# Optimization experiments

Hardware: AMD Instinct MI355X
Metric: run time of the kernel (lower is better)

The kernel has to match this reference:

```python
import jax, jax.numpy as jnp
import numpy as np

NUM_NODES = 19
RESOLUTION = 256
K_KNN = 3
EDGE_TOP_PERC = 0.5
RESIDUAL_W = 0.1
HIDDEN = 128
INPUT_DIM = 32


def _w(k, shape, fan):
    return jax.random.normal(k, shape, jnp.float32) / np.sqrt(fan)


def setup_inputs() -> dict:
    key = jax.random.key(0)
    ks = jax.random.split(key, 12)
    D, H = INPUT_DIM, HIDDEN
    return {
        "x": jax.random.normal(ks[0], (16 * NUM_NODES, 2048, D), jnp.float32),
        # GRU layer 0 (pytorch gate order r,z,n)
        "Wih0": _w(ks[1], (3 * H, D), D), "Whh0": _w(ks[2], (3 * H, H), H),
        "bih0": jnp.zeros(3 * H, jnp.float32), "bhh0": jnp.zeros(3 * H, jnp.float32),
        # GRU layer 1
        "Wih1": _w(ks[3], (3 * H, H), H), "Whh1": _w(ks[4], (3 * H, H), H),
        "bih1": jnp.zeros(3 * H, jnp.float32), "bhh1": jnp.zeros(3 * H, jnp.float32),
        # self-attention graph learner
        "Wq": _w(ks[5], (H, H), H), "Wk": _w(ks[6], (H, H), H),
        # SAGEConv: lin_l (neighbors, with bias) + lin_r (root)
        "Wl": _w(ks[7], (H, H), H), "Wr": _w(ks[8], (H, H), H),
        "b_sage": jnp.zeros(H, jnp.float32),
        # classifier
        "Wc": _w(ks[9], (1, H), H), "bc": jnp.zeros(1, jnp.float32),
    }


def gru_layer(x, Wih, Whh, bih, bhh):
    """x: (B,T,D) -> (B,T,H), pytorch nn.GRU gate order (r,z,n)."""
    H = Whh.shape[1]

    def step(h, xt):
        gi = xt @ Wih.T + bih          # (B,3H)
        gh = h @ Whh.T + bhh
        i_r, i_z, i_n = jnp.split(gi, 3, axis=-1)
        h_r, h_z, h_n = jnp.split(gh, 3, axis=-1)
        r = jax.nn.sigmoid(i_r + h_r)
        z = jax.nn.sigmoid(i_z + h_z)
        n = jnp.tanh(i_n + r * h_n)
        h_new = (1.0 - z) * n + z * h
        return h_new, h_new

    h0 = jnp.zeros((x.shape[0], H), x.dtype)
    _, ys = jax.lax.scan(step, h0, jnp.swapaxes(x, 0, 1))
    return jnp.swapaxes(ys, 0, 1)


def graphs4mer_forward(x, Wih0, Whh0, bih0, bhh0, Wih1, Whh1, bih1, bhh1,
                       Wq, Wk, Wl, Wr, b_sage, Wc, bc):
    B_total, T, _ = x.shape
    batch = B_total // NUM_NODES
    # temporal model: 2-layer GRU
    h = gru_layer(x, Wih0, Whh0, bih0, bhh0)
    h = gru_layer(h, Wih1, Whh1, bih1, bhh1)
    H = h.shape[-1]
    num_dyn = T // RESOLUTION
    # (batch, N, T, H) -> mean over each resolution window -> (batch, num_dyn, N, H)
    h = h.reshape(batch, NUM_NODES, num_dyn, RESOLUTION, H).mean(axis=3)
    xg = jnp.transpose(h, (0, 2, 1, 3)).reshape(batch * num_dyn, NUM_NODES, H)

    Bp, N = xg.shape[0], NUM_NODES
    I = jnp.eye(N, dtype=xg.dtype)

    # --- KNN cosine graph ---
    xn = xg / jnp.linalg.norm(xg, axis=-1, keepdims=True)
    sim = jnp.einsum('bnd,bmd->bnm', xn, xn)
    knn_val, knn_ind = jax.lax.top_k(sim, K_KNN)
    bi = jnp.arange(Bp)[:, None, None]
    ri = jnp.arange(N)[None, :, None]
    adj_knn = jnp.zeros_like(sim).at[bi, ri, knn_ind].set(knn_val)
    adj_knn = jnp.maximum(adj_knn, 0.0)
    adj_knn = (adj_knn + adj_knn.swapaxes(1, 2)) * 0.5   # undirected
    adj_knn = adj_knn * (1.0 - I) + I                    # force diag = 1

    # --- self-attention graph learner ---
    q = xg @ Wq.T
    k = xg @ Wk.T
    attn = jax.nn.softmax(jnp.einsum('bnd,bmd->bnm', q, k) / np.sqrt(H).astype(np.float32), axis=-1)
    attn = (attn + attn.swapaxes(1, 2)) * 0.5

    adj = RESIDUAL_W * adj_knn + (1.0 - RESIDUAL_W) * attn

    # --- prune: keep top edge_top_perc of entries per graph ---
    Kcut = int(N * N * EDGE_TOP_PERC)
    sorted_desc = -jnp.sort(-adj.reshape(Bp, -1), axis=-1)
    thr = sorted_desc[:, Kcut][:, None, None]
    adj = jnp.where(adj > thr, adj, 0.0)

    # --- feature smoothing regularization: tr(X^T L X)/F^2 ---
    d = adj.sum(-1)
    dis = jnp.where(d > 0, d ** -0.5, 0.0)
    L = I - dis[:, :, None] * adj * dis[:, None, :]
    mat = jnp.einsum('bnf,bnm,bmg->bfg', xg, L, xg) / float(H ** 2)
    reg = jnp.einsum('bff->b', mat).mean()

    # --- GraphSAGE conv on pruned graph (self loops removed, mean aggregation) ---
    adj_ns = adj * (1.0 - I)
    mask = (adj_ns > 0).astype(xg.dtype)
    deg = jnp.maximum(mask.sum(-1, keepdims=True), 1.0)
    agg = jnp.einsum('bnm,bmd->bnd', mask, xg) / deg
    out = jax.nn.relu(agg @ Wl.T + b_sage + xg @ Wr.T)

    # temporal mean pool over dynamic graphs, sum pool over nodes, classify
    out = out.reshape(batch, num_dyn, N, H).mean(axis=1).sum(axis=1)
    logits = out @ Wc.T + bc
    return logits, reg


def reference(x, Wih0, Whh0, bih0, bhh0, Wih1, Whh1, bih1, bhh1,
              Wq, Wk, Wl, Wr, b_sage, Wc, bc):
    return graphs4mer_forward(x, Wih0, Whh0, bih0, bhh0, Wih1, Whh1, bih1, bhh1,
                              Wq, Wk, Wl, Wr, b_sage, Wc, bc)
```

## Files before the change

### kernel.cpp

```cpp
#include <hip/hip_runtime.h>
#include <hip/hip_bf16.h>


#define NSEQ   304
#define TT     2048
#define HH     128
#define NNODE  19
#define NDYN   8
#define NGRAPH 128
#define NBLK   76

typedef __bf16 bf16x8 __attribute__((ext_vector_type(8)));
typedef float  f32x4  __attribute__((ext_vector_type(4)));

static __device__ __forceinline__ f32x4 mfma16(bf16x8 a, bf16x8 b, f32x4 c) {
  return __builtin_amdgcn_mfma_f32_16x16x32_bf16(a, b, c, 0, 0, 0);
}

static __device__ __forceinline__ float gate_step(
    float cr, float cz, float cn, float cm,
    float nBr, float nBz, float bin, float bhn, float hp)
{
  const float er = __builtin_amdgcn_exp2f(__builtin_fmaf(cr, -1.4426950408889634f, nBr));
  const float ez = __builtin_amdgcn_exp2f(__builtin_fmaf(cz, -1.4426950408889634f, nBz));
  const float r  = __builtin_amdgcn_rcpf(1.f + er);
  const float z  = __builtin_amdgcn_rcpf(1.f + ez);
  const float gn = __builtin_fmaf(r, cm + bhn, cn + bin);
  const float en = __builtin_amdgcn_exp2f(gn * 2.8853900817779268f);
  const float nn = __builtin_fmaf(__builtin_amdgcn_rcpf(1.f + en), -2.f, 1.f);
  return __builtin_fmaf(z, hp - nn, nn);
}

__global__ void wprep_kernel(const float* __restrict__ src, __bf16* __restrict__ dst,
                             int K, int nk)
{
  const int i = blockIdx.x * 256 + threadIdx.x;
  const int total = 8 * 3 * nk * 64;
  if (i >= total) return;
  const int l = i & 63;
  int rest = i >> 6;
  const int kc = rest % nk; rest /= nk;
  const int gs = rest % 3;
  const int w  = rest / 3;
  const int row = 128 * gs + 16 * w + (l & 15);
  const float* s = src + (size_t)row * K + kc * 32 + (l >> 4) * 8;
  bf16x8 v;
  #pragma unroll
  for (int u = 0; u < 8; ++u) v[u] = (__bf16)s[u];
  *(bf16x8*)&dst[(size_t)i * 8] = v;
}

__global__ void xprep_kernel(const float* __restrict__ x, __bf16* __restrict__ xb)
{
  const int i = blockIdx.x * 256 + threadIdx.x;
  if (i >= NNODE * TT * 64) return;
  const int l = i & 63;
  const int t = (i >> 6) & (TT - 1);
  const int g = i >> 17;
  const float* s = x + ((size_t)(g * 16 + (l & 15)) * TT + t) * 32 + (l >> 4) * 8;
  bf16x8 v;
  #pragma unroll
  for (int u = 0; u < 8; ++u) v[u] = (__bf16)s[u];
  *(bf16x8*)&xb[(size_t)i * 8] = v;
}

#define STEP_BARRIER() do {                                          \
    asm volatile("s_waitcnt lgkmcnt(0)" ::: "memory");               \
    __builtin_amdgcn_s_barrier();                                    \
    __builtin_amdgcn_sched_barrier(0);                               \
  } while (0)

template<int Q0>
static __device__ __forceinline__ void gru_body(
    const __bf16* __restrict__ xb,
    const __bf16* __restrict__ wI0, const __bf16* __restrict__ wH0,
    const __bf16* __restrict__ wI1, const __bf16* __restrict__ wH1,
    const float* __restrict__ bih0, const float* __restrict__ bhh0,
    const float* __restrict__ bih1, const float* __restrict__ bhh1,
    float* __restrict__ xg,
    __bf16* s0a, __bf16* s0b, __bf16* s1a, __bf16* s1b, int gg)
{
  const int tid = threadIdx.x;
  const int w   = tid >> 6;
  const int l   = tid & 63;
  const int lm  = l & 15;
  const int lq  = l >> 4;
  const int j   = 16 * w + lm;
  const f32x4 z4 = {0.f, 0.f, 0.f, 0.f};

  bf16x8 bI0[3], bH0[3][4], bI1[3][4], bH1[3][4];
  #pragma unroll
  for (int gs = 0; gs < 3; ++gs)
    bI0[gs] = *(const bf16x8*)&wI0[(size_t)((w * 3 + gs) * 64 + l) * 8];
  #pragma unroll
  for (int gs = 0; gs < 3; ++gs)
    #pragma unroll
    for (int kc = 0; kc < 4; ++kc) {
      const size_t fi = (size_t)(((w * 3 + gs) * 4 + kc) * 64 + l) * 8;
      bH0[gs][kc] = *(const bf16x8*)&wH0[fi];
      bI1[gs][kc] = *(const bf16x8*)&wI1[fi];
      bH1[gs][kc] = *(const bf16x8*)&wH1[fi];
    }

  const float L2E = 1.4426950408889634f;
  const float nBr0 = -L2E * (bih0[j] + bhh0[j]);
  const float nBz0 = -L2E * (bih0[128 + j] + bhh0[128 + j]);
  const float bin0 = bih0[256 + j], bhn0 = bhh0[256 + j];
  const float nBr1 = -L2E * (bih1[j] + bhh1[j]);
  const float nBz1 = -L2E * (bih1[128 + j] + bhh1[128 + j]);
  const float bin1 = bih1[256 + j], bhn1 = bhh1[256 + j];

  for (int i = tid; i < 16 * HH; i += 512) {
    s0a[i] = (__bf16)0.f; s0b[i] = (__bf16)0.f;
    s1a[i] = (__bf16)0.f; s1b[i] = (__bf16)0.f;
  }

  const int sw = lm & 7;
  int eo[4];
  #pragma unroll
  for (int kc = 0; kc < 4; ++kc)
    eo[kc] = lm * HH + ((((kc << 2) | lq) ^ sw) << 3);

  const int myrow = lq * 4 + Q0;
  const int woff  = myrow * HH + (((j >> 3) ^ (myrow & 7)) << 3) + (j & 7);
  const int seq   = gg * 16 + myrow;
  const int bidx  = seq / NNODE;
  const int node  = seq - bidx * NNODE;

  float h0p = 0.f, h1p = 0.f, hsum = 0.f;

  const __bf16* xrow = xb + (size_t)gg * TT * 512 + l * 8;
  bf16x8 a0 = *(const bf16x8*)xrow;
  __syncthreads();

  for (int t = 0; t < TT; ++t) {
    __bf16*       h0w = (t & 1) ? s0b : s0a;
    const __bf16* h0r = (t & 1) ? s0a : s0b;
    __bf16*       h1w = (t & 1) ? s1a : s1b;
    const __bf16* h1r = (t & 1) ? s1b : s1a;

    bf16x8 a0n = *(const bf16x8*)(xrow + (size_t)((t + 1) & (TT - 1)) * 512);

    bf16x8 ah0[4], ah1[4];
    #pragma unroll
    for (int kc = 0; kc < 4; ++kc) ah0[kc] = *(const bf16x8*)&h0r[eo[kc]];
    #pragma unroll
    for (int kc = 0; kc < 4; ++kc) ah1[kc] = *(const bf16x8*)&h1r[eo[kc]];

    f32x4 Cr = mfma16(a0, bI0[0], z4);
    f32x4 Cz = mfma16(a0, bI0[1], z4);
    f32x4 Cn = mfma16(a0, bI0[2], z4);

    f32x4 Dr = z4, Dz = z4, Dn = z4, Dm = z4;
    if (t > 0) {
      #pragma unroll
      for (int kc = 0; kc < 4; ++kc) {
        Dr = mfma16(ah0[kc], bI1[0][kc], Dr);
        Dz = mfma16(ah0[kc], bI1[1][kc], Dz);
        Dn = mfma16(ah0[kc], bI1[2][kc], Dn);
      }
      #pragma unroll
      for (int kc = 0; kc < 4; ++kc) {
        Dr = mfma16(ah1[kc], bH1[0][kc], Dr);
        Dz = mfma16(ah1[kc], bH1[1][kc], Dz);
        Dm = mfma16(ah1[kc], bH1[2][kc], Dm);
      }
    }

    f32x4 Cm = z4;
    #pragma unroll
    for (int kc = 0; kc < 4; ++kc) {
      Cr = mfma16(ah0[kc], bH0[0][kc], Cr);
      Cz = mfma16(ah0[kc], bH0[1][kc], Cz);
      Cm = mfma16(ah0[kc], bH0[2][kc], Cm);
    }

    if (t > 0) {
      const float h = gate_step(Dr[Q0], Dz[Q0], Dn[Q0], Dm[Q0],
                                nBr1, nBz1, bin1, bhn1, h1p);
      h1p = h;
      hsum += h;
      h1w[woff] = (__bf16)h;
      const int s = t - 1;
      if ((s & 255) == 255) {
        const int win = s >> 8;
        xg[((size_t)(bidx * NDYN + win) * NNODE + node) * HH + j] =
            hsum * (1.f / 256.f);
        hsum = 0.f;
      }
    }
    {
      const float h = gate_step(Cr[Q0], Cz[Q0], Cn[Q0], Cm[Q0],
                                nBr0, nBz0, bin0, bhn0, h0p);
      h0p = h;
      h0w[woff] = (__bf16)h;
    }
    a0 = a0n;
    STEP_BARRIER();
  }

  {
    const __bf16* h0r = s0b;
    const __bf16* h1r = s1a;
    bf16x8 ah0[4], ah1[4];
    #pragma unroll
    for (int kc = 0; kc < 4; ++kc) ah0[kc] = *(const bf16x8*)&h0r[eo[kc]];
    #pragma unroll
    for (int kc = 0; kc < 4; ++kc) ah1[kc] = *(const bf16x8*)&h1r[eo[kc]];
    f32x4 Dr = z4, Dz = z4, Dn = z4, Dm = z4;
    #pragma unroll
    for (int kc = 0; kc < 4; ++kc) {
      Dr = mfma16(ah0[kc], bI1[0][kc], Dr);
      Dz = mfma16(ah0[kc], bI1[1][kc], Dz);
      Dn = mfma16(ah0[kc], bI1[2][kc], Dn);
    }
    #pragma unroll
    for (int kc = 0; kc < 4; ++kc) {
      Dr = mfma16(ah1[kc], bH1[0][kc], Dr);
      Dz = mfma16(ah1[kc], bH1[1][kc], Dz);
      Dm = mfma16(ah1[kc], bH1[2][kc], Dm);
    }
    const float h = gate_step(Dr[Q0], Dz[Q0], Dn[Q0], Dm[Q0],
                              nBr1, nBz1, bin1, bhn1, h1p);
    hsum += h;
    xg[((size_t)(bidx * NDYN + 7) * NNODE + node) * HH + j] =
        hsum * (1.f / 256.f);
  }
}

__global__ __launch_bounds__(512) __attribute__((amdgpu_waves_per_eu(2, 2)))
void gru2_kernel(
    const __bf16* __restrict__ xb,
    const __bf16* __restrict__ wI0, const __bf16* __restrict__ wH0,
    const __bf16* __restrict__ wI1, const __bf16* __restrict__ wH1,
    const float* __restrict__ bih0, const float* __restrict__ bhh0,
    const float* __restrict__ bih1, const float* __restrict__ bhh1,
    float* __restrict__ xg)
{
  __shared__ __align__(16) __bf16 sH0[2][16 * HH];
  __shared__ __align__(16) __bf16 sH1[2][16 * HH];
  const int gg = blockIdx.x >> 2;
  switch (blockIdx.x & 3) {
    case 0: gru_body<0>(xb, wI0, wH0, wI1, wH1, bih0, bhh0, bih1, bhh1, xg,
                        sH0[0], sH0[1], sH1[0], sH1[1], gg); break;
    case 1: gru_body<1>(xb, wI0, wH0, wI1, wH1, bih0, bhh0, bih1, bhh1, xg,
                        sH0[0], sH0[1], sH1[0], sH1[1], gg); break;
    case 2: gru_body<2>(xb, wI0, wH0, wI1, wH1, bih0, bhh0, bih1, bhh1, xg,
                        sH0[0], sH0[1], sH1[0], sH1[1], gg); break;
    default: gru_body<3>(xb, wI0, wH0, wI1, wH1, bih0, bhh0, bih1, bhh1, xg,
                         sH0[0], sH0[1], sH1[0], sH1[1], gg); break;
  }
}

static __device__ __forceinline__ float blockReduce256(float v, float* sRed)
{
  const int tid = threadIdx.x;
  __syncthreads();
  sRed[tid] = v;
  __syncthreads();
  #pragma unroll
  for (int st = 128; st >= 1; st >>= 1) {
    if (tid < st) sRed[tid] += sRed[tid + st];
    __syncthreads();
  }
  return sRed[0];
}

__global__ __launch_bounds__(256) void graph_kernel(
    const float* __restrict__ xg,
    const float* __restrict__ Wq, const float* __restrict__ Wk,
    const float* __restrict__ Wl, const float* __restrict__ Wr,
    const float* __restrict__ bs, const float* __restrict__ Wc,
    float* __restrict__ out)
{
  const int tid = threadIdx.x;
  const int bp = blockIdx.x;

  __shared__ float sX[NNODE * HH];
  __shared__ float sQ[NNODE * HH];
  __shared__ float sK[NNODE * HH];
  __shared__ float sG[NNODE * NNODE];
  __shared__ float sA[NNODE * NNODE];
  __shared__ float sS[NNODE * NNODE];
  __shared__ float sNorm[NNODE];
  __shared__ float sDis[NNODE];
  __shared__ float sDeg[NNODE];
  __shared__ float sThr;
  __shared__ float sRed[256];

  for (int idx = tid; idx < NNODE * HH; idx += 256)
    sX[idx] = xg[(size_t)bp * NNODE * HH + idx];
  __syncthreads();

  if (tid < NNODE) {
    float acc = 0.f;
    const float* xv = &sX[tid * HH];
    #pragma unroll 4
    for (int d = 0; d < HH; ++d) acc += xv[d] * xv[d];
    sNorm[tid] = 1.f / sqrtf(acc);
  }
  for (int e = tid; e < NNODE * NNODE; e += 256) {
    const int n = e / NNODE, m = e % NNODE;
    float acc = 0.f;
    const float* a = &sX[n * HH];
    const float* b = &sX[m * HH];
    #pragma unroll 4
    for (int d = 0; d < HH; ++d) acc += a[d] * b[d];
    sG[e] = acc;
  }
  for (int e = tid; e < NNODE * NNODE; e += 256) sA[e] = 0.f;
  __syncthreads();

  if (tid < NNODE) {
    const int r = tid;
    const float nr = sNorm[r];
    float v0 = -1e30f, v1 = -1e30f, v2 = -1e30f;
    int i0 = 0, i1 = 0, i2 = 0;
    for (int m = 0; m < NNODE; ++m) {
      const float v = sG[r * NNODE + m] * nr * sNorm[m];
      if (v > v0)      { v2 = v1; i2 = i1; v1 = v0; i1 = i0; v0 = v; i0 = m; }
      else if (v > v1) { v2 = v1; i2 = i1; v1 = v;  i1 = m; }
      else if (v > v2) { v2 = v;  i2 = m; }
    }
    sA[r * NNODE + i0] = fmaxf(v0, 0.f);
    sA[r * NNODE + i1] = fmaxf(v1, 0.f);
    sA[r * NNODE + i2] = fmaxf(v2, 0.f);
  }
  __syncthreads();

  {
    float t0 = 0.f, t1 = 0.f;
    if (tid < 361) {
      const int n = tid / NNODE, m = tid % NNODE;
      t0 = (n == m) ? 1.f : 0.5f * (sA[n * NNODE + m] + sA[m * NNODE + n]);
    }
    if (tid + 256 < 361) {
      const int e = tid + 256;
      const int n = e / NNODE, m = e % NNODE;
      t1 = (n == m) ? 1.f : 0.5f * (sA[n * NNODE + m] + sA[m * NNODE + n]);
    }
    __syncthreads();
    if (tid < 361) sA[tid] = t0;
    if (tid + 256 < 361) sA[tid + 256] = t1;
  }

  for (int o = tid; o < NNODE * HH; o += 256) {
    const int n = o >> 7, hh = o & 127;
    float aq = 0.f, ak = 0.f;
    const float* xv = &sX[n * HH];
    const float* wq = &Wq[hh * HH];
    const float* wk = &Wk[hh * HH];
    #pragma unroll 4
    for (int d = 0; d < HH; ++d) { const float xx = xv[d]; aq += xx * wq[d]; ak += xx * wk[d]; }
    sQ[o] = aq; sK[o] = ak;
  }
  __syncthreads();

  for (int e = tid; e < NNODE * NNODE; e += 256) {
    const int n = e / NNODE, m = e % NNODE;
    float acc = 0.f;
    const float* a = &sQ[n * HH];
    const float* b = &sK[m * HH];
    #pragma unroll 4
    for (int d = 0; d < HH; ++d) acc += a[d] * b[d];
    sS[e] = acc * 0.08838834764831845f;
  }
  __syncthreads();
  if (tid < NNODE) {
    const int r = tid;
    float mx = -1e30f;
    for (int m = 0; m < NNODE; ++m) mx = fmaxf(mx, sS[r * NNODE + m]);
    float sum = 0.f;
    for (int m = 0; m < NNODE; ++m) sum += expf(sS[r * NNODE + m] - mx);
    const float inv = 1.f / sum;
    for (int m = 0; m < NNODE; ++m)
      sS[r * NNODE + m] = expf(sS[r * NNODE + m] - mx) * inv;
  }
  __syncthreads();

  for (int e = tid; e < NNODE * NNODE; e += 256) {
    const int n = e / NNODE, m = e % NNODE;
    sA[e] = 0.1f * sA[e] + 0.45f * (sS[n * NNODE + m] + sS[m * NNODE + n]);
  }
  __syncthreads();

  for (int e = tid; e < NNODE * NNODE; e += 256) {
    const float v = sA[e];
    int cg = 0, ce = 0;
    for (int f = 0; f < NNODE * NNODE; ++f) {
      const float u = sA[f];
      cg += (u > v);
      ce += (u == v);
    }
    if (cg <= 180 && cg + ce > 180) sThr = v;
  }
  __syncthreads();
  {
    const float thr = sThr;
    for (int e = tid; e < NNODE * NNODE; e += 256)
      sA[e] = (sA[e] > thr) ? sA[e] : 0.f;
  }
  __syncthreads();

  if (tid < NNODE) {
    const int r = tid;
    float dsum = 0.f;
    int cnt = 0;
    for (int m = 0; m < NNODE; ++m) {
      const float v = sA[r * NNODE + m];
      dsum += v;
      if (m != r && v > 0.f) ++cnt;
    }
    sDis[r] = (dsum > 0.f) ? 1.f / sqrtf(dsum) : 0.f;
    sDeg[r] = (float)(cnt < 1 ? 1 : cnt);
  }
  __syncthreads();

  float regp = 0.f;
  for (int e = tid; e < NNODE * NNODE; e += 256) {
    const int n = e / NNODE, m = e % NNODE;
    const float Lnm = ((n == m) ? 1.f : 0.f) - sDis[n] * sDis[m] * sA[e];
    regp += Lnm * sG[e];
  }
  {
    const float tr = blockReduce256(regp, sRed);
    if (tid == 0)
      atomicAdd(out + 16, tr * (1.f / (16384.f * (float)NGRAPH)));
  }
  __syncthreads();

  for (int o = tid; o < NNODE * HH; o += 256) {
    const int n = o >> 7, d = o & 127;
    float acc = 0.f;
    for (int m = 0; m < NNODE; ++m)
      if (m != n && sA[n * NNODE + m] > 0.f) acc += sX[m * HH + d];
    sQ[o] = acc / sDeg[n];
  }
  __syncthreads();

  float lgp = 0.f;
  for (int o = tid; o < NNODE * HH; o += 256) {
    const int n = o >> 7, hh = o & 127;
    float acc = bs[hh];
    const float* av = &sQ[n * HH];
    const float* xv = &sX[n * HH];
    const float* wl = &Wl[hh * HH];
    const float* wr = &Wr[hh * HH];
    #pragma unroll 4
    for (int d = 0; d < HH; ++d) acc += av[d] * wl[d] + xv[d] * wr[d];
    lgp += fmaxf(acc, 0.f) * Wc[hh];
  }
  {
    const float tot = blockReduce256(lgp, sRed);
    if (tid == 0)
      atomicAdd(out + (bp >> 3), tot * 0.125f);
  }
}

__global__ void init_out_kernel(float* __restrict__ out, const float* __restrict__ bc)
{
  const int i = threadIdx.x;
  if (i < 16) out[i] = bc[0];
  else if (i == 16) out[16] = 0.f;
}

extern "C" void kernel_launch(void* const* d_in, const int* in_sizes, int n_in,
                              void* d_out, int out_size, void* d_ws, size_t ws_size,
                              hipStream_t stream)
{
  const float* x    = (const float*)d_in[0];
  const float* Wih0 = (const float*)d_in[1];
  const float* Whh0 = (const float*)d_in[2];
  const float* bih0 = (const float*)d_in[3];
  const float* bhh0 = (const float*)d_in[4];
  const float* Wih1 = (const float*)d_in[5];
  const float* Whh1 = (const float*)d_in[6];
  const float* bih1 = (const float*)d_in[7];
  const float* bhh1 = (const float*)d_in[8];
  const float* Wq   = (const float*)d_in[9];
  const float* Wk   = (const float*)d_in[10];
  const float* Wl   = (const float*)d_in[11];
  const float* Wr   = (const float*)d_in[12];
  const float* bsg  = (const float*)d_in[13];
  const float* Wc   = (const float*)d_in[14];
  const float* bc   = (const float*)d_in[15];
  float* out = (float*)d_out;

  const size_t XB  = (size_t)NNODE * TT * 512 * sizeof(__bf16);
  const size_t WI0 = (size_t)8 * 3 * 64 * 8 * sizeof(__bf16);
  const size_t WH  = (size_t)8 * 3 * 4 * 64 * 8 * sizeof(__bf16);
  char* p = (char*)d_ws;
  __bf16* xb  = (__bf16*)p;            p += XB;
  __bf16* wI0 = (__bf16*)p;            p += WI0;
  __bf16* wH0 = (__bf16*)p;            p += WH;
  __bf16* wI1 = (__bf16*)p;            p += WH;
  __bf16* wH1 = (__bf16*)p;            p += WH;
  float*  xg  = (float*)p;

  init_out_kernel<<<1, 64, 0, stream>>>(out, bc);
  wprep_kernel<<<6, 256, 0, stream>>>(Wih0, wI0, 32, 1);
  wprep_kernel<<<24, 256, 0, stream>>>(Whh0, wH0, 128, 4);
  wprep_kernel<<<24, 256, 0, stream>>>(Whh1, wH1, 128, 4);
  wprep_kernel<<<24, 256, 0, stream>>>(Wih1, wI1, 128, 4);
  xprep_kernel<<<(NNODE * TT * 64 + 255) / 256, 256, 0, stream>>>(x, xb);
  gru2_kernel<<<NBLK, 512, 0, stream>>>(
      xb, wI0, wH0, wI1, wH1, bih0, bhh0, bih1, bhh1, xg);
  graph_kernel<<<NGRAPH, 256, 0, stream>>>(xg, Wq, Wk, Wl, Wr, bsg, Wc, out);
}
```

Measured before the change: 2.055 ms.

## Halve GRU block to 4 waves, each handling two hidden-column chunks

The GRU recurrence block shrinks from 8 waves to 4, with each wave now owning two 16-column slices of the hidden dimension and holding twice as many weight fragments in registers. Empty asm statements pin the weights in VGPRs, and launch bounds are set to one wave per EU. The goal is to cut per-step barrier cost and raise per-wave MFMA work to hide latency in the serial time loop. The cost is doubled register pressure, possible spills, and half as many waves in flight per step.

```diff
diff --git a/kernel.cpp b/kernel.cpp
--- a/kernel.cpp
+++ b/kernel.cpp
@@ -85,32 +85,54 @@
   const int l   = tid & 63;
   const int lm  = l & 15;
   const int lq  = l >> 4;
-  const int j   = 16 * w + lm;
   const f32x4 z4 = {0.f, 0.f, 0.f, 0.f};
 
-  bf16x8 bI0[3], bH0[3][4], bI1[3][4], bH1[3][4];
-  #pragma unroll
-  for (int gs = 0; gs < 3; ++gs)
-    bI0[gs] = *(const bf16x8*)&wI0[(size_t)((w * 3 + gs) * 64 + l) * 8];
-  #pragma unroll
-  for (int gs = 0; gs < 3; ++gs)
-    #pragma unroll
-    for (int kc = 0; kc < 4; ++kc) {
-      const size_t fi = (size_t)(((w * 3 + gs) * 4 + kc) * 64 + l) * 8;
-      bH0[gs][kc] = *(const bf16x8*)&wH0[fi];
-      bI1[gs][kc] = *(const bf16x8*)&wI1[fi];
-      bH1[gs][kc] = *(const bf16x8*)&wH1[fi];
+  bf16x8 bI0[2][3], bH0[2][3][4], bI1[2][3][4], bH1[2][3][4];
+  #pragma unroll
+  for (int c = 0; c < 2; ++c) {
+    const int wb = w + 4 * c;
+    #pragma unroll
+    for (int gs = 0; gs < 3; ++gs)
+      bI0[c][gs] = *(const bf16x8*)&wI0[(size_t)((wb * 3 + gs) * 64 + l) * 8];
+    #pragma unroll
+    for (int gs = 0; gs < 3; ++gs)
+      #pragma unroll
+      for (int kc = 0; kc < 4; ++kc) {
+        const size_t fi = (size_t)(((wb * 3 + gs) * 4 + kc) * 64 + l) * 8;
+        bH0[c][gs][kc] = *(const bf16x8*)&wH0[fi];
+        bI1[c][gs][kc] = *(const bf16x8*)&wI1[fi];
+        bH1[c][gs][kc] = *(const bf16x8*)&wH1[fi];
+      }
+  }
+  #pragma unroll
+  for (int c = 0; c < 2; ++c)
+    #pragma unroll
+    for (int gs = 0; gs < 3; ++gs) {
+      asm volatile("" : "+v"(bI0[c][gs]));
+      #pragma unroll
+      for (int kc = 0; kc < 4; ++kc) {
+        asm volatile("" : "+v"(bH0[c][gs][kc]));
+        asm volatile("" : "+v"(bI1[c][gs][kc]));
+        asm volatile("" : "+v"(bH1[c][gs][kc]));
+      }
     }
 
   const float L2E = 1.4426950408889634f;
-  const float nBr0 = -L2E * (bih0[j] + bhh0[j]);
-  const float nBz0 = -L2E * (bih0[128 + j] + bhh0[128 + j]);
-  const float bin0 = bih0[256 + j], bhn0 = bhh0[256 + j];
-  const float nBr1 = -L2E * (bih1[j] + bhh1[j]);
-  const float nBz1 = -L2E * (bih1[128 + j] + bhh1[128 + j]);
-  const float bin1 = bih1[256 + j], bhn1 = bhh1[256 + j];
-
-  for (int i = tid; i < 16 * HH; i += 512) {
+  int jc[2];
+  float nBr0[2], nBz0[2], bin0[2], bhn0[2], nBr1[2], nBz1[2], bin1[2], bhn1[2];
+  #pragma unroll
+  for (int c = 0; c < 2; ++c) {
+    const int j = 16 * w + lm + 64 * c;
+    jc[c] = j;
+    nBr0[c] = -L2E * (bih0[j] + bhh0[j]);
+    nBz0[c] = -L2E * (bih0[128 + j] + bhh0[128 + j]);
+    bin0[c] = bih0[256 + j]; bhn0[c] = bhh0[256 + j];
+    nBr1[c] = -L2E * (bih1[j] + bhh1[j]);
+    nBz1[c] = -L2E * (bih1[128 + j] + bhh1[128 + j]);
+    bin1[c] = bih1[256 + j]; bhn1[c] = bhh1[256 + j];
+  }
+
+  for (int i = tid; i < 16 * HH; i += 256) {
     s0a[i] = (__bf16)0.f; s0b[i] = (__bf16)0.f;
     s1a[i] = (__bf16)0.f; s1b[i] = (__bf16)0.f;
   }
@@ -122,12 +144,15 @@
     eo[kc] = lm * HH + ((((kc << 2) | lq) ^ sw) << 3);
 
   const int myrow = lq * 4 + Q0;
-  const int woff  = myrow * HH + (((j >> 3) ^ (myrow & 7)) << 3) + (j & 7);
+  int woff[2];
+  #pragma unroll
+  for (int c = 0; c < 2; ++c)
+    woff[c] = myrow * HH + (((jc[c] >> 3) ^ (myrow & 7)) << 3) + (jc[c] & 7);
   const int seq   = gg * 16 + myrow;
   const int bidx  = seq / NNODE;
   const int node  = seq - bidx * NNODE;
 
-  float h0p = 0.f, h1p = 0.f, hsum = 0.f;
+  float h0p[2] = {0.f, 0.f}, h1p[2] = {0.f, 0.f}, hsum[2] = {0.f, 0.f};
 
   const __bf16* xrow = xb + (size_t)gg * TT * 512 + l * 8;
   bf16x8 a0 = *(const bf16x8*)xrow;
@@ -147,53 +172,69 @@
     #pragma unroll
     for (int kc = 0; kc < 4; ++kc) ah1[kc] = *(const bf16x8*)&h1r[eo[kc]];
 
-    f32x4 Cr = mfma16(a0, bI0[0], z4);
-    f32x4 Cz = mfma16(a0, bI0[1], z4);
-    f32x4 Cn = mfma16(a0, bI0[2], z4);
-
-    f32x4 Dr = z4, Dz = z4, Dn = z4, Dm = z4;
+    f32x4 Cr[2], Cz[2], Cn[2], Cm[2], Dr[2], Dz[2], Dn[2], Dm[2];
+    #pragma unroll
+    for (int c = 0; c < 2; ++c) {
+      Cr[c] = mfma16(a0, bI0[c][0], z4);
+      Cz[c] = mfma16(a0, bI0[c][1], z4);
+      Cn[c] = mfma16(a0, bI0[c][2], z4);
+      Cm[c] = z4; Dr[c] = z4; Dz[c] = z4; Dn[c] = z4; Dm[c] = z4;
+    }
+
     if (t > 0) {
       #pragma unroll
-      for (int kc = 0; kc < 4; ++kc) {
-        Dr = mfma16(ah0[kc], bI1[0][kc], Dr);
-        Dz = mfma16(ah0[kc], bI1[1][kc], Dz);
-        Dn = mfma16(ah0[kc], bI1[2][kc], Dn);
-      }
-      #pragma unroll
-      for (int kc = 0; kc < 4; ++kc) {
-        Dr = mfma16(ah1[kc], bH1[0][kc], Dr);
-        Dz = mfma16(ah1[kc], bH1[1][kc], Dz);
-        Dm = mfma16(ah1[kc], bH1[2][kc], Dm);
-      }
-    }
-
-    f32x4 Cm = z4;
-    #pragma unroll
-    for (int kc = 0; kc < 4; ++kc) {
-      Cr = mfma16(ah0[kc], bH0[0][kc], Cr);
-      Cz = mfma16(ah0[kc], bH0[1][kc], Cz);
-      Cm = mfma16(ah0[kc], bH0[2][kc], Cm);
-    }
+      for (int kc = 0; kc < 4; ++kc)
+        #pragma unroll
+        for (int c = 0; c < 2; ++c) {
+          Dr[c] = mfma16(ah0[kc], bI1[c][0][kc], Dr[c]);
+          Dz[c] = mfma16(ah0[kc], bI1[c][1][kc], Dz[c]);
+          Dn[c] = mfma16(ah0[kc], bI1[c][2][kc], Dn[c]);
+        }
+      #pragma unroll
+      for (int kc = 0; kc < 4; ++kc)
+        #pragma unroll
+        for (int c = 0; c < 2; ++c) {
+          Dr[c] = mfma16(ah1[kc], bH1[c][0][kc], Dr[c]);
+          Dz[c] = mfma16(ah1[kc], bH1[c][1][kc], Dz[c]);
+          Dm[c] = mfma16(ah1[kc], bH1[c][2][kc], Dm[c]);
+        }
+    }
+
+    #pragma unroll
+    for (int kc = 0; kc < 4; ++kc)
+      #pragma unroll
+      for (int c = 0; c < 2; ++c) {
+        Cr[c] = mfma16(ah0[kc], bH0[c][0][kc], Cr[c]);
+        Cz[c] = mfma16(ah0[kc], bH0[c][1][kc], Cz[c]);
+        Cm[c] = mfma16(ah0[kc], bH0[c][2][kc], Cm[c]);
+      }
 
     if (t > 0) {
-      const float h = gate_step(Dr[Q0], Dz[Q0], Dn[Q0], Dm[Q0],
-                                nBr1, nBz1, bin1, bhn1, h1p);
-      h1p = h;
-      hsum += h;
-      h1w[woff] = (__bf16)h;
+      #pragma unroll
+      for (int c = 0; c < 2; ++c) {
+        const float h = gate_step(Dr[c][Q0], Dz[c][Q0], Dn[c][Q0], Dm[c][Q0],
+                                  nBr1[c], nBz1[c], bin1[c], bhn1[c], h1p[c]);
+        h1p[c] = h;
+        hsum[c] += h;
+        h1w[woff[c]] = (__bf16)h;
+      }
       const int s = t - 1;
       if ((s & 255) == 255) {
         const int win = s >> 8;
-        xg[((size_t)(bidx * NDYN + win) * NNODE + node) * HH + j] =
-            hsum * (1.f / 256.f);
-        hsum = 0.f;
-      }
-    }
-    {
-      const float h = gate_step(Cr[Q0], Cz[Q0], Cn[Q0], Cm[Q0],
-                                nBr0, nBz0, bin0, bhn0, h0p);
-      h0p = h;
-      h0w[woff] = (__bf16)h;
+        #pragma unroll
+        for (int c = 0; c < 2; ++c) {
+          xg[((size_t)(bidx * NDYN + win) * NNODE + node) * HH + jc[c]] =
+              hsum[c] * (1.f / 256.f);
+          hsum[c] = 0.f;
+        }
+      }
+    }
+    #pragma unroll
+    for (int c = 0; c < 2; ++c) {
+      const float h = gate_step(Cr[c][Q0], Cz[c][Q0], Cn[c][Q0], Cm[c][Q0],
+                                nBr0[c], nBz0[c], bin0[c], bhn0[c], h0p[c]);
+      h0p[c] = h;
+      h0w[woff[c]] = (__bf16)h;
     }
     a0 = a0n;
     STEP_BARRIER();
@@ -207,28 +248,37 @@
     for (int kc = 0; kc < 4; ++kc) ah0[kc] = *(const bf16x8*)&h0r[eo[kc]];
     #pragma unroll
     for (int kc = 0; kc < 4; ++kc) ah1[kc] = *(const bf16x8*)&h1r[eo[kc]];
-    f32x4 Dr = z4, Dz = z4, Dn = z4, Dm = z4;
-    #pragma unroll
-    for (int kc = 0; kc < 4; ++kc) {
-      Dr = mfma16(ah0[kc], bI1[0][kc], Dr);
-      Dz = mfma16(ah0[kc], bI1[1][kc], Dz);
-      Dn = mfma16(ah0[kc], bI1[2][kc], Dn);
-    }
-    #pragma unroll
-    for (int kc = 0; kc < 4; ++kc) {
-      Dr = mfma16(ah1[kc], bH1[0][kc], Dr);
-      Dz = mfma16(ah1[kc], bH1[1][kc], Dz);
-      Dm = mfma16(ah1[kc], bH1[2][kc], Dm);
-    }
-    const float h = gate_step(Dr[Q0], Dz[Q0], Dn[Q0], Dm[Q0],
-                              nBr1, nBz1, bin1, bhn1, h1p);
-    hsum += h;
-    xg[((size_t)(bidx * NDYN + 7) * NNODE + node) * HH + j] =
-        hsum * (1.f / 256.f);
-  }
-}
-
-__global__ __launch_bounds__(512) __attribute__((amdgpu_waves_per_eu(2, 2)))
+    f32x4 Dr[2], Dz[2], Dn[2], Dm[2];
+    #pragma unroll
+    for (int c = 0; c < 2; ++c) { Dr[c] = z4; Dz[c] = z4; Dn[c] = z4; Dm[c] = z4; }
+    #pragma unroll
+    for (int kc = 0; kc < 4; ++kc)
+      #pragma unroll
+      for (int c = 0; c < 2; ++c) {
+        Dr[c] = mfma16(ah0[kc], bI1[c][0][kc], Dr[c]);
+        Dz[c] = mfma16(ah0[kc], bI1[c][1][kc], Dz[c]);
+        Dn[c] = mfma16(ah0[kc], bI1[c][2][kc], Dn[c]);
+      }
+    #pragma unroll
+    for (int kc = 0; kc < 4; ++kc)
+      #pragma unroll
+      for (int c = 0; c < 2; ++c) {
+        Dr[c] = mfma16(ah1[kc], bH1[c][0][kc], Dr[c]);
+        Dz[c] = mfma16(ah1[kc], bH1[c][1][kc], Dz[c]);
+        Dm[c] = mfma16(ah1[kc], bH1[c][2][kc], Dm[c]);
+      }
+    #pragma unroll
+    for (int c = 0; c < 2; ++c) {
+      const float h = gate_step(Dr[c][Q0], Dz[c][Q0], Dn[c][Q0], Dm[c][Q0],
+                                nBr1[c], nBz1[c], bin1[c], bhn1[c], h1p[c]);
+      hsum[c] += h;
+      xg[((size_t)(bidx * NDYN + 7) * NNODE + node) * HH + jc[c]] =
+          hsum[c] * (1.f / 256.f);
+    }
+  }
+}
+
+__global__ __launch_bounds__(256, 1) __attribute__((amdgpu_waves_per_eu(1, 1)))
 void gru2_kernel(
     const __bf16* __restrict__ xb,
     const __bf16* __restrict__ wI0, const __bf16* __restrict__ wH0,
@@ -503,7 +553,7 @@
   wprep_kernel<<<24, 256, 0, stream>>>(Whh1, wH1, 128, 4);
   wprep_kernel<<<24, 256, 0, stream>>>(Wih1, wI1, 128, 4);
   xprep_kernel<<<(NNODE * TT * 64 + 255) / 256, 256, 0, stream>>>(x, xb);
-  gru2_kernel<<<NBLK, 512, 0, stream>>>(
+  gru2_kernel<<<NBLK, 256, 0, stream>>>(
       xb, wI0, wH0, wI1, wH1, bih0, bhh0, bih1, bhh1, xg);
   graph_kernel<<<NGRAPH, 256, 0, stream>>>(xg, Wq, Wk, Wl, Wr, bsg, Wc, out);
 }
```

New measurement: 2.629 ms. +27.9%, slower.

## Process two independent row chains per GRU block and compact hidden-state LDS

Applied to the files above, without the earlier changes.

Each GRU block now advances two independent sequence subsets (Q offsets A and B) instead of one, halving the block count from 76 to 38. The input projection MFMAs are shared between the two chains, and their interleaved recurrences give the scheduler independent work to hide MFMA and LDS latency within each serial timestep. Hidden-state LDS buffers shrink to 4 rows with a padded pitch and a new XOR swizzle. The trade-off is twice the per-step work on each block and fewer blocks across the CUs.

```diff
diff --git a/kernel.cpp b/kernel.cpp
--- a/kernel.cpp
+++ b/kernel.cpp
@@ -8,7 +8,8 @@
 #define NNODE  19
 #define NDYN   8
 #define NGRAPH 128
-#define NBLK   76
+#define NBLK   38
+#define CPITCH 160
 
 typedef __bf16 bf16x8 __attribute__((ext_vector_type(8)));
 typedef float  f32x4  __attribute__((ext_vector_type(4)));
@@ -71,15 +72,109 @@
   } while (0)
 
 template<int Q0>
-static __device__ __forceinline__ void gru_body(
+static __device__ __forceinline__ void gru_step(
+    const int t, const f32x4 Cxr, const f32x4 Cxz, const f32x4 Cxn,
+    const __bf16* h0r, __bf16* h0w, const __bf16* h1r, __bf16* h1w,
+    const bf16x8 (*bH0)[4], const bf16x8 (*bI1)[4], const bf16x8 (*bH1)[4],
+    const int* eo, const int woff,
+    const float nBr0, const float nBz0, const float bin0, const float bhn0,
+    const float nBr1, const float nBz1, const float bin1, const float bhn1,
+    float& h0p, float& h1p, float& hsum, float* __restrict__ xgbase)
+{
+  const f32x4 z4 = {0.f, 0.f, 0.f, 0.f};
+  bf16x8 ah0[4], ah1[4];
+  #pragma unroll
+  for (int kc = 0; kc < 4; ++kc) ah0[kc] = *(const bf16x8*)&h0r[eo[kc]];
+  #pragma unroll
+  for (int kc = 0; kc < 4; ++kc) ah1[kc] = *(const bf16x8*)&h1r[eo[kc]];
+
+  f32x4 Dr = z4, Dz = z4, Dn = z4, Dm = z4;
+  if (t > 0) {
+    #pragma unroll
+    for (int kc = 0; kc < 4; ++kc) {
+      Dr = mfma16(ah0[kc], bI1[0][kc], Dr);
+      Dz = mfma16(ah0[kc], bI1[1][kc], Dz);
+      Dn = mfma16(ah0[kc], bI1[2][kc], Dn);
+    }
+    #pragma unroll
+    for (int kc = 0; kc < 4; ++kc) {
+      Dr = mfma16(ah1[kc], bH1[0][kc], Dr);
+      Dz = mfma16(ah1[kc], bH1[1][kc], Dz);
+      Dm = mfma16(ah1[kc], bH1[2][kc], Dm);
+    }
+  }
+
+  f32x4 Cr = Cxr, Cz = Cxz, Cn = Cxn, Cm = z4;
+  #pragma unroll
+  for (int kc = 0; kc < 4; ++kc) {
+    Cr = mfma16(ah0[kc], bH0[0][kc], Cr);
+    Cz = mfma16(ah0[kc], bH0[1][kc], Cz);
+    Cm = mfma16(ah0[kc], bH0[2][kc], Cm);
+  }
+
+  if (t > 0) {
+    const float h = gate_step(Dr[Q0], Dz[Q0], Dn[Q0], Dm[Q0],
+                              nBr1, nBz1, bin1, bhn1, h1p);
+    h1p = h;
+    hsum += h;
+    h1w[woff] = (__bf16)h;
+    const int s = t - 1;
+    if ((s & 255) == 255) {
+      xgbase[(size_t)(s >> 8) * (NNODE * HH)] = hsum * (1.f / 256.f);
+      hsum = 0.f;
+    }
+  }
+  {
+    const float h = gate_step(Cr[Q0], Cz[Q0], Cn[Q0], Cm[Q0],
+                              nBr0, nBz0, bin0, bhn0, h0p);
+    h0p = h;
+    h0w[woff] = (__bf16)h;
+  }
+}
+
+template<int Q0>
+static __device__ __forceinline__ void gru_epilogue(
+    const __bf16* h0r, const __bf16* h1r,
+    const bf16x8 (*bI1)[4], const bf16x8 (*bH1)[4],
+    const int* eo,
+    const float nBr1, const float nBz1, const float bin1, const float bhn1,
+    float h1p, float hsum, float* __restrict__ xgbase)
+{
+  const f32x4 z4 = {0.f, 0.f, 0.f, 0.f};
+  bf16x8 ah0[4], ah1[4];
+  #pragma unroll
+  for (int kc = 0; kc < 4; ++kc) ah0[kc] = *(const bf16x8*)&h0r[eo[kc]];
+  #pragma unroll
+  for (int kc = 0; kc < 4; ++kc) ah1[kc] = *(const bf16x8*)&h1r[eo[kc]];
+  f32x4 Dr = z4, Dz = z4, Dn = z4, Dm = z4;
+  #pragma unroll
+  for (int kc = 0; kc < 4; ++kc) {
+    Dr = mfma16(ah0[kc], bI1[0][kc], Dr);
+    Dz = mfma16(ah0[kc], bI1[1][kc], Dz);
+    Dn = mfma16(ah0[kc], bI1[2][kc], Dn);
+  }
+  #pragma unroll
+  for (int kc = 0; kc < 4; ++kc) {
+    Dr = mfma16(ah1[kc], bH1[0][kc], Dr);
+    Dz = mfma16(ah1[kc], bH1[1][kc], Dz);
+    Dm = mfma16(ah1[kc], bH1[2][kc], Dm);
+  }
+  const float h = gate_step(Dr[Q0], Dz[Q0], Dn[Q0], Dm[Q0],
+                            nBr1, nBz1, bin1, bhn1, h1p);
+  hsum += h;
+  xgbase[(size_t)7 * (NNODE * HH)] = hsum * (1.f / 256.f);
+}
+
+template<int QA>
+static __device__ __forceinline__ void gru_pair(
     const __bf16* __restrict__ xb,
     const __bf16* __restrict__ wI0, const __bf16* __restrict__ wH0,
     const __bf16* __restrict__ wI1, const __bf16* __restrict__ wH1,
     const float* __restrict__ bih0, const float* __restrict__ bhh0,
     const float* __restrict__ bih1, const float* __restrict__ bhh1,
-    float* __restrict__ xg,
-    __bf16* s0a, __bf16* s0b, __bf16* s1a, __bf16* s1b, int gg)
-{
+    float* __restrict__ xg, __bf16* S, int gg)
+{
+  constexpr int QB = QA + 1;
   const int tid = threadIdx.x;
   const int w   = tid >> 6;
   const int l   = tid & 63;
@@ -88,6 +183,15 @@
   const int j   = 16 * w + lm;
   const f32x4 z4 = {0.f, 0.f, 0.f, 0.f};
 
+  __bf16* s0aA = S + 0 * (4 * CPITCH);
+  __bf16* s0bA = S + 1 * (4 * CPITCH);
+  __bf16* s1aA = S + 2 * (4 * CPITCH);
+  __bf16* s1bA = S + 3 * (4 * CPITCH);
+  __bf16* s0aB = S + 4 * (4 * CPITCH);
+  __bf16* s0bB = S + 5 * (4 * CPITCH);
+  __bf16* s1aB = S + 6 * (4 * CPITCH);
+  __bf16* s1bB = S + 7 * (4 * CPITCH);
+
   bf16x8 bI0[3], bH0[3][4], bI1[3][4], bH1[3][4];
   #pragma unroll
   for (int gs = 0; gs < 3; ++gs)
@@ -110,122 +214,67 @@
   const float nBz1 = -L2E * (bih1[128 + j] + bhh1[128 + j]);
   const float bin1 = bih1[256 + j], bhn1 = bhh1[256 + j];
 
-  for (int i = tid; i < 16 * HH; i += 512) {
-    s0a[i] = (__bf16)0.f; s0b[i] = (__bf16)0.f;
-    s1a[i] = (__bf16)0.f; s1b[i] = (__bf16)0.f;
-  }
-
-  const int sw = lm & 7;
+  for (int i = tid; i < 8 * 4 * CPITCH; i += 512) S[i] = (__bf16)0.f;
+
+  const int rr = lm >> 2;
   int eo[4];
   #pragma unroll
   for (int kc = 0; kc < 4; ++kc)
-    eo[kc] = lm * HH + ((((kc << 2) | lq) ^ sw) << 3);
-
-  const int myrow = lq * 4 + Q0;
-  const int woff  = myrow * HH + (((j >> 3) ^ (myrow & 7)) << 3) + (j & 7);
-  const int seq   = gg * 16 + myrow;
-  const int bidx  = seq / NNODE;
-  const int node  = seq - bidx * NNODE;
-
-  float h0p = 0.f, h1p = 0.f, hsum = 0.f;
+    eo[kc] = rr * CPITCH + ((((kc << 2) | lq) ^ rr) << 3);
+  const int woff = lq * CPITCH + (((j >> 3) ^ lq) << 3) + (j & 7);
+
+  const int myrowA = lq * 4 + QA;
+  const int seqA   = gg * 16 + myrowA;
+  const int bidxA  = seqA / NNODE;
+  const int nodeA  = seqA - bidxA * NNODE;
+  float* xgbaseA = xg + ((size_t)(bidxA * NDYN) * NNODE + nodeA) * HH + j;
+  const int myrowB = lq * 4 + QB;
+  const int seqB   = gg * 16 + myrowB;
+  const int bidxB  = seqB / NNODE;
+  const int nodeB  = seqB - bidxB * NNODE;
+  float* xgbaseB = xg + ((size_t)(bidxB * NDYN) * NNODE + nodeB) * HH + j;
+
+  float h0pA = 0.f, h1pA = 0.f, hsumA = 0.f;
+  float h0pB = 0.f, h1pB = 0.f, hsumB = 0.f;
 
   const __bf16* xrow = xb + (size_t)gg * TT * 512 + l * 8;
   bf16x8 a0 = *(const bf16x8*)xrow;
   __syncthreads();
 
   for (int t = 0; t < TT; ++t) {
-    __bf16*       h0w = (t & 1) ? s0b : s0a;
-    const __bf16* h0r = (t & 1) ? s0a : s0b;
-    __bf16*       h1w = (t & 1) ? s1a : s1b;
-    const __bf16* h1r = (t & 1) ? s1b : s1a;
+    const bool p = (t & 1) != 0;
+    __bf16*       h0wA = p ? s0bA : s0aA;
+    const __bf16* h0rA = p ? s0aA : s0bA;
+    __bf16*       h1wA = p ? s1aA : s1bA;
+    const __bf16* h1rA = p ? s1bA : s1aA;
+    __bf16*       h0wB = p ? s0bB : s0aB;
+    const __bf16* h0rB = p ? s0aB : s0bB;
+    __bf16*       h1wB = p ? s1aB : s1bB;
+    const __bf16* h1rB = p ? s1bB : s1aB;
 
     bf16x8 a0n = *(const bf16x8*)(xrow + (size_t)((t + 1) & (TT - 1)) * 512);
 
-    bf16x8 ah0[4], ah1[4];
-    #pragma unroll
-    for (int kc = 0; kc < 4; ++kc) ah0[kc] = *(const bf16x8*)&h0r[eo[kc]];
-    #pragma unroll
-    for (int kc = 0; kc < 4; ++kc) ah1[kc] = *(const bf16x8*)&h1r[eo[kc]];
-
-    f32x4 Cr = mfma16(a0, bI0[0], z4);
-    f32x4 Cz = mfma16(a0, bI0[1], z4);
-    f32x4 Cn = mfma16(a0, bI0[2], z4);
-
-    f32x4 Dr = z4, Dz = z4, Dn = z4, Dm = z4;
-    if (t > 0) {
-      #pragma unroll
-      for (int kc = 0; kc < 4; ++kc) {
-        Dr = mfma16(ah0[kc], bI1[0][kc], Dr);
-        Dz = mfma16(ah0[kc], bI1[1][kc], Dz);
-        Dn = mfma16(ah0[kc], bI1[2][kc], Dn);
-      }
-      #pragma unroll
-      for (int kc = 0; kc < 4; ++kc) {
-        Dr = mfma16(ah1[kc], bH1[0][kc], Dr);
-        Dz = mfma16(ah1[kc], bH1[1][kc], Dz);
-        Dm = mfma16(ah1[kc], bH1[2][kc], Dm);
-      }
-    }
-
-    f32x4 Cm = z4;
-    #pragma unroll
-    for (int kc = 0; kc < 4; ++kc) {
-      Cr = mfma16(ah0[kc], bH0[0][kc], Cr);
-      Cz = mfma16(ah0[kc], bH0[1][kc], Cz);
-      Cm = mfma16(ah0[kc], bH0[2][kc], Cm);
-    }
-
-    if (t > 0) {
-      const float h = gate_step(Dr[Q0], Dz[Q0], Dn[Q0], Dm[Q0],
-                                nBr1, nBz1, bin1, bhn1, h1p);
-      h1p = h;
-      hsum += h;
-      h1w[woff] = (__bf16)h;
-      const int s = t - 1;
-      if ((s & 255) == 255) {
-        const int win = s >> 8;
-        xg[((size_t)(bidx * NDYN + win) * NNODE + node) * HH + j] =
-            hsum * (1.f / 256.f);
-        hsum = 0.f;
-      }
-    }
-    {
-      const float h = gate_step(Cr[Q0], Cz[Q0], Cn[Q0], Cm[Q0],
-                                nBr0, nBz0, bin0, bhn0, h0p);
-      h0p = h;
-      h0w[woff] = (__bf16)h;
-    }
+    f32x4 Cxr = mfma16(a0, bI0[0], z4);
+    f32x4 Cxz = mfma16(a0, bI0[1], z4);
+    f32x4 Cxn = mfma16(a0, bI0[2], z4);
+
+    gru_step<QA>(t, Cxr, Cxz, Cxn, h0rA, h0wA, h1rA, h1wA,
+                 bH0, bI1, bH1, eo, woff,
+                 nBr0, nBz0, bin0, bhn0, nBr1, nBz1, bin1, bhn1,
+                 h0pA, h1pA, hsumA, xgbaseA);
+    gru_step<QB>(t, Cxr, Cxz, Cxn, h0rB, h0wB, h1rB, h1wB,
+                 bH0, bI1, bH1, eo, woff,
+                 nBr0, nBz0, bin0, bhn0, nBr1, nBz1, bin1, bhn1,
+                 h0pB, h1pB, hsumB, xgbaseB);
+
     a0 = a0n;
     STEP_BARRIER();
   }
 
-  {
-    const __bf16* h0r = s0b;
-    const __bf16* h1r = s1a;
-    bf16x8 ah0[4], ah1[4];
-    #pragma unroll
-    for (int kc = 0; kc < 4; ++kc) ah0[kc] = *(const bf16x8*)&h0r[eo[kc]];
-    #pragma unroll
-    for (int kc = 0; kc < 4; ++kc) ah1[kc] = *(const bf16x8*)&h1r[eo[kc]];
-    f32x4 Dr = z4, Dz = z4, Dn = z4, Dm = z4;
-    #pragma unroll
-    for (int kc = 0; kc < 4; ++kc) {
-      Dr = mfma16(ah0[kc], bI1[0][kc], Dr);
-      Dz = mfma16(ah0[kc], bI1[1][kc], Dz);
-      Dn = mfma16(ah0[kc], bI1[2][kc], Dn);
-    }
-    #pragma unroll
-    for (int kc = 0; kc < 4; ++kc) {
-      Dr = mfma16(ah1[kc], bH1[0][kc], Dr);
-      Dz = mfma16(ah1[kc], bH1[1][kc], Dz);
-      Dm = mfma16(ah1[kc], bH1[2][kc], Dm);
-    }
-    const float h = gate_step(Dr[Q0], Dz[Q0], Dn[Q0], Dm[Q0],
-                              nBr1, nBz1, bin1, bhn1, h1p);
-    hsum += h;
-    xg[((size_t)(bidx * NDYN + 7) * NNODE + node) * HH + j] =
-        hsum * (1.f / 256.f);
-  }
+  gru_epilogue<QA>(s0bA, s1aA, bI1, bH1, eo, nBr1, nBz1, bin1, bhn1,
+                   h1pA, hsumA, xgbaseA);
+  gru_epilogue<QB>(s0bB, s1aB, bI1, bH1, eo, nBr1, nBz1, bin1, bhn1,
+                   h1pB, hsumB, xgbaseB);
 }
 
 __global__ __launch_bounds__(512) __attribute__((amdgpu_waves_per_eu(2, 2)))
@@ -237,19 +286,12 @@
     const float* __restrict__ bih1, const float* __restrict__ bhh1,
     float* __restrict__ xg)
 {
-  __shared__ __align__(16) __bf16 sH0[2][16 * HH];
-  __shared__ __align__(16) __bf16 sH1[2][16 * HH];
-  const int gg = blockIdx.x >> 2;
-  switch (blockIdx.x & 3) {
-    case 0: gru_body<0>(xb, wI0, wH0, wI1, wH1, bih0, bhh0, bih1, bhh1, xg,
-                        sH0[0], sH0[1], sH1[0], sH1[1], gg); break;
-    case 1: gru_body<1>(xb, wI0, wH0, wI1, wH1, bih0, bhh0, bih1, bhh1, xg,
-                        sH0[0], sH0[1], sH1[0], sH1[1], gg); break;
-    case 2: gru_body<2>(xb, wI0, wH0, wI1, wH1, bih0, bhh0, bih1, bhh1, xg,
-                        sH0[0], sH0[1], sH1[0], sH1[1], gg); break;
-    default: gru_body<3>(xb, wI0, wH0, wI1, wH1, bih0, bhh0, bih1, bhh1, xg,
-                         sH0[0], sH0[1], sH1[0], sH1[1], gg); break;
-  }
+  __shared__ __align__(16) __bf16 S[8 * 4 * CPITCH];
+  const int gg = blockIdx.x >> 1;
+  if (blockIdx.x & 1)
+    gru_pair<2>(xb, wI0, wH0, wI1, wH1, bih0, bhh0, bih1, bhh1, xg, S, gg);
+  else
+    gru_pair<0>(xb, wI0, wH0, wI1, wH1, bih0, bhh0, bih1, bhh1, xg, S, gg);
 }
 
 static __device__ __forceinline__ float blockReduce256(float v, float* sRed)
```

Result: slower. 3.436 ms (+67.2%).
